# Kernel optimization log

Measured on AMD Instinct MI355X. Metric: run time of the kernel, lower is better.

Reference implementation:

```python
import jax, jax.numpy as jnp
import numpy as np

N_NODES = 100000


def gcn_conv(x, edge_index, W, b):
    # PyG GCNConv: add self-loops, symmetric norm, then scatter-aggregate.
    n = x.shape[0]
    x = x @ W  # [N, out]
    src = jnp.concatenate([edge_index[0], jnp.arange(n)])  # self-loops
    dst = jnp.concatenate([edge_index[1], jnp.arange(n)])
    ones = jnp.ones(src.shape[0], dtype=x.dtype)
    deg = jax.ops.segment_sum(ones, dst, num_segments=n)  # in-degree incl. self-loops
    dis = jnp.where(deg > 0, jax.lax.rsqrt(deg), 0.0)
    norm = dis[src] * dis[dst]  # [E+N]
    msg = x[src] * norm[:, None]  # gather + scale
    out = jax.ops.segment_sum(msg, dst, num_segments=n)
    return out + b


def setup_inputs() -> dict:
    key = jax.random.key(0)
    ks = jax.random.split(key, 8)
    in_dim, h1, h2, out_dim, E = 128, 128, 64, 10, 1600000
    glorot = lambda k, fi, fo: jax.random.normal(k, (fi, fo), jnp.float32) * np.sqrt(2.0 / (fi + fo))
    return {
        "x": jax.random.normal(ks[0], (N_NODES, in_dim), jnp.float32),
        "edge_index": jax.random.randint(ks[1], (2, E), 0, N_NODES, jnp.int64),
        "W1": glorot(ks[2], in_dim, h1),
        "b1": jnp.zeros((h1,), jnp.float32),
        "W2": glorot(ks[3], h1, h2),
        "b2": jnp.zeros((h2,), jnp.float32),
        "Wf": glorot(ks[4], h2, out_dim),
        "bf": jnp.zeros((out_dim,), jnp.float32),
    }


def reference(x, edge_index, W1, b1, W2, b2, Wf, bf):
    h = jax.nn.relu(gcn_conv(x, edge_index, W1, b1))
    h = jax.nn.relu(gcn_conv(h, edge_index, W2, b2))
    logits = h @ Wf + bf
    return jax.nn.softmax(logits, axis=1)
```

## Files before the change

### kernel.cpp

```cpp
#include <hip/hip_runtime.h>
#include <math.h>

#define NN 100000
#define D_IN 128
#define D_H1 128
#define D_H2 64
#define D_O 10
#define NB 256
#define BDIV 391
#define ECH 2048
#define COLCAP 8192

static const size_t OFF_G1     = 0;
static const size_t OFF_G2     = 25600000;
static const size_t OFF_PART   = 76800000;
static const size_t OFF_COL    = 102400000;
static const size_t OFF_DIS    = 108800000;
static const size_t OFF_ROWPTR = 109300000;
static const size_t OFF_HIST   = 109800000;
static const size_t OFF_TOT    = 110700000;
static const size_t OFF_BASE   = 110710000;

typedef __attribute__((ext_vector_type(8))) short short8;
typedef __attribute__((ext_vector_type(4))) float floatx4;

__device__ inline unsigned int pack_bf2(float a, float b) {
  unsigned int ua = __float_as_uint(a);
  ua += 0x7fffu + ((ua >> 16) & 1u);
  unsigned int ub = __float_as_uint(b);
  ub += 0x7fffu + ((ub >> 16) & 1u);
  return (ua >> 16) | (ub & 0xffff0000u);
}
__device__ inline unsigned short bf16u(float a) {
  unsigned int ua = __float_as_uint(a);
  ua += 0x7fffu + ((ua >> 16) & 1u);
  return (unsigned short)(ua >> 16);
}
__device__ inline float bflo(unsigned int u) { return __uint_as_float(u << 16); }
__device__ inline float bfhi(unsigned int u) { return __uint_as_float(u & 0xffff0000u); }
__device__ inline short8 as_short8(uint4 u) {
  union { uint4 u4; short8 s8; } c; c.u4 = u; return c.s8;
}
__device__ inline void acc_u4(float* acc, uint4 u) {
  acc[0] += bflo(u.x); acc[1] += bfhi(u.x);
  acc[2] += bflo(u.y); acc[3] += bfhi(u.y);
  acc[4] += bflo(u.z); acc[5] += bfhi(u.z);
  acc[6] += bflo(u.w); acc[7] += bfhi(u.w);
}

__global__ __launch_bounds__(256) void histo_kernel(
    const int* __restrict__ dst, int* __restrict__ H, int E, int nchunk) {
  __shared__ int hist[NB];
  const int tid = threadIdx.x;
  hist[tid] = 0;
  __syncthreads();
  const int e0 = blockIdx.x * ECH;
#pragma unroll
  for (int i = 0; i < ECH / 256; ++i) {
    int e = e0 + i * 256 + tid;
    if (e < E) atomicAdd(&hist[dst[e] / BDIV], 1);
  }
  __syncthreads();
  H[tid * nchunk + blockIdx.x] = hist[tid];
}

__global__ __launch_bounds__(256) void bucket_scan_kernel(
    int* __restrict__ H, int* __restrict__ total, int nchunk) {
  __shared__ int sm[256];
  const int tid = threadIdx.x;
  int* row = H + (size_t)blockIdx.x * nchunk;
  int carry = 0;
  for (int t0 = 0; t0 < nchunk; t0 += 256) {
    int idx = t0 + tid;
    int v = (idx < nchunk) ? row[idx] : 0;
    sm[tid] = v;
    __syncthreads();
#pragma unroll
    for (int off = 1; off < 256; off <<= 1) {
      int t2 = (tid >= off) ? sm[tid - off] : 0;
      __syncthreads();
      sm[tid] += t2;
      __syncthreads();
    }
    int incl = sm[tid];
    int ttot = sm[255];
    __syncthreads();
    if (idx < nchunk) row[idx] = carry + incl - v;
    carry += ttot;
  }
  if (tid == 0) total[blockIdx.x] = carry;
}

__global__ __launch_bounds__(256) void base_scan_kernel(
    const int* __restrict__ total, int* __restrict__ base) {
  __shared__ int sm[256];
  const int tid = threadIdx.x;
  int v = total[tid];
  sm[tid] = v;
  __syncthreads();
#pragma unroll
  for (int off = 1; off < 256; off <<= 1) {
    int t2 = (tid >= off) ? sm[tid - off] : 0;
    __syncthreads();
    sm[tid] += t2;
    __syncthreads();
  }
  base[tid] = sm[tid] - v;
  if (tid == 255) base[256] = sm[255];
}

__global__ __launch_bounds__(256) void scatter_kernel(
    const int* __restrict__ src, const int* __restrict__ dst,
    const int* __restrict__ H, const int* __restrict__ base,
    int2* __restrict__ part, int E, int nchunk) {
  __shared__ int offs_s[NB];
  __shared__ int base_s[NB];
  __shared__ int cnt[NB];
  const int tid = threadIdx.x;
  offs_s[tid] = H[tid * nchunk + blockIdx.x];
  base_s[tid] = base[tid];
  cnt[tid] = 0;
  __syncthreads();
  const int e0 = blockIdx.x * ECH;
#pragma unroll
  for (int i = 0; i < ECH / 256; ++i) {
    int e = e0 + i * 256 + tid;
    if (e < E) {
      int d = dst[e];
      int s = src[e];
      int b = d / BDIV;
      int r = atomicAdd(&cnt[b], 1);
      part[(size_t)base_s[b] + offs_s[b] + r] = make_int2(d, s);
    }
  }
}

__global__ __launch_bounds__(256) void bucket_csr_kernel(
    const int2* __restrict__ part, const int* __restrict__ base,
    int* __restrict__ row_ptr, float* __restrict__ dis,
    int* __restrict__ col, int n, int E) {
  __shared__ int sm[256];
  __shared__ int ldeg[BDIV + 1];
  __shared__ int lofs[BDIV + 1];
  __shared__ int col_s[COLCAP];
  const int tid = threadIdx.x;
  const int b = blockIdx.x;
  const int lo = b * BDIV;
  const int nn = min(n - lo, BDIV);
  const int ebase = base[b];
  const int ecnt = base[b + 1] - ebase;

  for (int t = tid; t <= BDIV; t += 256) ldeg[t] = 0;
  __syncthreads();
  for (int i0 = 0; i0 < ecnt; i0 += 256) {
    int idx = i0 + tid;
    if (idx < ecnt) atomicAdd(&ldeg[part[ebase + idx].x - lo], 1);
  }
  __syncthreads();
  int carry = 0;
  for (int t0 = 0; t0 < BDIV + 1; t0 += 256) {
    int idx = t0 + tid;
    int v = (idx <= BDIV) ? ldeg[idx] : 0;
    sm[tid] = v;
    __syncthreads();
#pragma unroll
    for (int off = 1; off < 256; off <<= 1) {
      int t2 = (tid >= off) ? sm[tid - off] : 0;
      __syncthreads();
      sm[tid] += t2;
      __syncthreads();
    }
    int incl = sm[tid];
    int ttot = sm[255];
    __syncthreads();
    if (idx <= BDIV) lofs[idx] = carry + incl - v;
    carry += ttot;
  }
  __syncthreads();
  for (int t = tid; t < nn; t += 256) {
    row_ptr[lo + t] = ebase + lofs[t];
    dis[lo + t] = rsqrtf((float)ldeg[t] + 1.0f);
  }
  if (b == NB - 1 && tid == 0) row_ptr[n] = E;
  __syncthreads();
  for (int i0 = 0; i0 < ecnt; i0 += 256) {
    int idx = i0 + tid;
    if (idx < ecnt) {
      int2 p = part[ebase + idx];
      int r = atomicAdd(&lofs[p.x - lo], 1);
      if (r < COLCAP) col_s[r] = p.y;
    }
  }
  __syncthreads();
  const int m = min(ecnt, COLCAP);
  for (int idx = tid; idx < m; idx += 256) col[ebase + idx] = col_s[idx];
}

template <int NOUT>
__global__ __launch_bounds__(256) void gemm_mfma_kernel(
    const float* __restrict__ A_, const float* __restrict__ W,
    const float* __restrict__ dis, unsigned short* __restrict__ out, int nrows) {
  constexpr int K = 128;
  constexpr int NT = NOUT / 16;
  constexpr int LDW = K + 8;
  __shared__ unsigned short wt[NOUT * LDW];
  __shared__ unsigned short buf[4 * 16 * LDW];
  const int tid = threadIdx.x;

  {
    constexpr int NGRP = 256 / NOUT;
    constexpr int KG = K / NGRP;
    int n = tid % NOUT;
    int k0 = (tid / NOUT) * KG;
#pragma unroll
    for (int kb = 0; kb < KG / 8; ++kb) {
      int k = k0 + kb * 8;
      unsigned int u0 = pack_bf2(W[(size_t)(k + 0) * NOUT + n], W[(size_t)(k + 1) * NOUT + n]);
      unsigned int u1 = pack_bf2(W[(size_t)(k + 2) * NOUT + n], W[(size_t)(k + 3) * NOUT + n]);
      unsigned int u2 = pack_bf2(W[(size_t)(k + 4) * NOUT + n], W[(size_t)(k + 5) * NOUT + n]);
      unsigned int u3 = pack_bf2(W[(size_t)(k + 6) * NOUT + n], W[(size_t)(k + 7) * NOUT + n]);
      *(uint4*)(wt + n * LDW + k) = make_uint4(u0, u1, u2, u3);
    }
  }

  const int wave = tid >> 6;
  const int lane = tid & 63;
  const int quad = lane >> 4;
  const int cg = lane & 15;
  const int row0w = blockIdx.x * 64 + wave * 16;

  short8 afr[4];
  {
    int row = row0w + cg;
    if (row > nrows - 1) row = nrows - 1;
#pragma unroll
    for (int kb = 0; kb < 4; ++kb) {
      const float* p = A_ + (size_t)row * K + kb * 32 + quad * 8;
      float4 v0 = *(const float4*)(p);
      float4 v1 = *(const float4*)(p + 4);
      uint4 u;
      u.x = pack_bf2(v0.x, v0.y); u.y = pack_bf2(v0.z, v0.w);
      u.z = pack_bf2(v1.x, v1.y); u.w = pack_bf2(v1.z, v1.w);
      afr[kb] = as_short8(u);
    }
  }
  __syncthreads();

  floatx4 acc[NT];
#pragma unroll
  for (int t = 0; t < NT; ++t) acc[t] = (floatx4){0.f, 0.f, 0.f, 0.f};
#pragma unroll
  for (int t = 0; t < NT; ++t) {
    const unsigned short* wrow = wt + (t * 16 + cg) * LDW;
#pragma unroll
    for (int kb = 0; kb < 4; ++kb) {
      short8 bfr = *(const short8*)(wrow + kb * 32 + quad * 8);
      acc[t] = __builtin_amdgcn_mfma_f32_16x16x32_bf16(afr[kb], bfr, acc[t], 0, 0, 0);
    }
  }

  float4 dv4 = *(const float4*)(dis + row0w + quad * 4);
  float dvs[4] = {dv4.x, dv4.y, dv4.z, dv4.w};
  unsigned short* mybuf = buf + wave * 16 * LDW;
#pragma unroll
  for (int t = 0; t < NT; ++t)
#pragma unroll
    for (int r = 0; r < 4; ++r)
      mybuf[(quad * 4 + r) * LDW + t * 16 + cg] = bf16u(acc[t][r] * dvs[r]);
  __syncthreads();

  constexpr int CHUNKS = NOUT / 8;
  constexpr int RPI = 64 / CHUNKS;
  int cid = lane % CHUNKS;
  int rs = lane / CHUNKS;
#pragma unroll
  for (int i = 0; i < 16 / RPI; ++i) {
    int r = rs + i * RPI;
    int grow = row0w + r;
    if (grow < nrows) {
      uint4 u = *(const uint4*)(mybuf + r * LDW + cid * 8);
      *(uint4*)(out + (size_t)grow * NOUT + cid * 8) = u;
    }
  }
}

__global__ __launch_bounds__(256) void gather1_gemm2_kernel(
    const unsigned short* __restrict__ g, const int* __restrict__ col,
    const int* __restrict__ row_ptr, const float* __restrict__ dis,
    const float* __restrict__ b1, const float* __restrict__ W2,
    unsigned short* __restrict__ g2, int n) {
  constexpr int K = D_H1;
  constexpr int LDW = K + 8;
  constexpr int LDO = 80;
  __shared__ unsigned short wt[D_H2 * LDW];
  __shared__ unsigned short hl[16 * LDW];
  __shared__ unsigned short obuf[16 * LDO];
  const int tid = threadIdx.x;
  const int row0 = blockIdx.x * 16;

  {
    int nn = tid & 63;
    int k0 = (tid >> 6) * 32;
#pragma unroll
    for (int kb = 0; kb < 4; ++kb) {
      int k = k0 + kb * 8;
      unsigned int u0 = pack_bf2(W2[(size_t)(k + 0) * D_H2 + nn], W2[(size_t)(k + 1) * D_H2 + nn]);
      unsigned int u1 = pack_bf2(W2[(size_t)(k + 2) * D_H2 + nn], W2[(size_t)(k + 3) * D_H2 + nn]);
      unsigned int u2 = pack_bf2(W2[(size_t)(k + 4) * D_H2 + nn], W2[(size_t)(k + 5) * D_H2 + nn]);
      unsigned int u3 = pack_bf2(W2[(size_t)(k + 6) * D_H2 + nn], W2[(size_t)(k + 7) * D_H2 + nn]);
      *(uint4*)(wt + nn * LDW + k) = make_uint4(u0, u1, u2, u3);
    }
  }

  {
    const int v = row0 + (tid >> 4);
    const int c = (tid & 15) * 8;
    const int start = row_ptr[v];
    const int end = row_ptr[v + 1];
    float acc[8];
#pragma unroll
    for (int q = 0; q < 8; ++q) acc[q] = 0.f;
    acc_u4(acc, *(const uint4*)(g + (size_t)v * K + c));
    int e = start;
    for (; e + 4 <= end; e += 4) {
      int s0 = col[e + 0], s1 = col[e + 1], s2 = col[e + 2], s3 = col[e + 3];
      uint4 u0 = *(const uint4*)(g + (size_t)s0 * K + c);
      uint4 u1 = *(const uint4*)(g + (size_t)s1 * K + c);
      uint4 u2 = *(const uint4*)(g + (size_t)s2 * K + c);
      uint4 u3 = *(const uint4*)(g + (size_t)s3 * K + c);
      acc_u4(acc, u0); acc_u4(acc, u1); acc_u4(acc, u2); acc_u4(acc, u3);
    }
    for (; e < end; ++e) {
      uint4 u = *(const uint4*)(g + (size_t)col[e] * K + c);
      acc_u4(acc, u);
    }
    float dv = dis[v];
    float4 bv0 = *(const float4*)(b1 + c);
    float4 bv1 = *(const float4*)(b1 + c + 4);
    float r0 = fmaxf(dv * acc[0] + bv0.x, 0.f);
    float r1 = fmaxf(dv * acc[1] + bv0.y, 0.f);
    float r2 = fmaxf(dv * acc[2] + bv0.z, 0.f);
    float r3 = fmaxf(dv * acc[3] + bv0.w, 0.f);
    float r4 = fmaxf(dv * acc[4] + bv1.x, 0.f);
    float r5 = fmaxf(dv * acc[5] + bv1.y, 0.f);
    float r6 = fmaxf(dv * acc[6] + bv1.z, 0.f);
    float r7 = fmaxf(dv * acc[7] + bv1.w, 0.f);
    uint4 o;
    o.x = pack_bf2(r0, r1);
    o.y = pack_bf2(r2, r3);
    o.z = pack_bf2(r4, r5);
    o.w = pack_bf2(r6, r7);
    *(uint4*)(hl + (tid >> 4) * LDW + c) = o;
  }
  __syncthreads();

  {
    const int wave = tid >> 6;
    const int lane = tid & 63;
    const int quad = lane >> 4;
    const int cg = lane & 15;
    floatx4 acc = (floatx4){0.f, 0.f, 0.f, 0.f};
    const unsigned short* wrow = wt + (wave * 16 + cg) * LDW;
    const unsigned short* arow = hl + cg * LDW;
#pragma unroll
    for (int kb = 0; kb < 4; ++kb) {
      short8 afr = *(const short8*)(arow + kb * 32 + quad * 8);
      short8 bfr = *(const short8*)(wrow + kb * 32 + quad * 8);
      acc = __builtin_amdgcn_mfma_f32_16x16x32_bf16(afr, bfr, acc, 0, 0, 0);
    }
    float4 dv4 = *(const float4*)(dis + row0 + quad * 4);
    float dvs[4] = {dv4.x, dv4.y, dv4.z, dv4.w};
#pragma unroll
    for (int r = 0; r < 4; ++r)
      obuf[(quad * 4 + r) * LDO + wave * 16 + cg] = bf16u(acc[r] * dvs[r]);
  }
  __syncthreads();

  if (tid < 128) {
    int r = tid >> 3;
    int cid = tid & 7;
    uint4 u = *(const uint4*)(obuf + r * LDO + cid * 8);
    *(uint4*)(g2 + (size_t)(row0 + r) * D_H2 + cid * 8) = u;
  }
}

__global__ __launch_bounds__(256) void gather2_final_kernel(
    const unsigned short* __restrict__ g, const int* __restrict__ col,
    const int* __restrict__ row_ptr, const float* __restrict__ dis,
    const float* __restrict__ b2, const float* __restrict__ Wf,
    const float* __restrict__ bf, float* __restrict__ out, int n) {
  constexpr int LDH = 72;
  __shared__ unsigned short ha[32 * LDH];
  __shared__ unsigned short wtf[16 * LDH];
  __shared__ float bfs[D_O];
  __shared__ float ls[32][12];
  const int tid = threadIdx.x;
  if (tid < 128) {
    int nn = tid >> 3;
    int k = (tid & 7) * 8;
    uint4 u;
    if (nn < D_O) {
      u.x = pack_bf2(Wf[(size_t)(k + 0) * D_O + nn], Wf[(size_t)(k + 1) * D_O + nn]);
      u.y = pack_bf2(Wf[(size_t)(k + 2) * D_O + nn], Wf[(size_t)(k + 3) * D_O + nn]);
      u.z = pack_bf2(Wf[(size_t)(k + 4) * D_O + nn], Wf[(size_t)(k + 5) * D_O + nn]);
      u.w = pack_bf2(Wf[(size_t)(k + 6) * D_O + nn], Wf[(size_t)(k + 7) * D_O + nn]);
    } else {
      u = make_uint4(0u, 0u, 0u, 0u);
    }
    *(uint4*)(wtf + nn * LDH + k) = u;
  }
  if (tid < D_O) bfs[tid] = bf[tid];

  const int gid = blockIdx.x * 256 + tid;
  const int v = gid >> 3;
  const int nl = tid >> 3;
  const int c = (tid & 7) * 8;
  if (v < n) {
    int start = row_ptr[v];
    int end = row_ptr[v + 1];
    float acc[8];
#pragma unroll
    for (int q = 0; q < 8; ++q) acc[q] = 0.f;
    acc_u4(acc, *(const uint4*)(g + (size_t)v * D_H2 + c));
    int e = start;
    for (; e + 4 <= end; e += 4) {
      int s0 = col[e + 0], s1 = col[e + 1], s2 = col[e + 2], s3 = col[e + 3];
      uint4 u0 = *(const uint4*)(g + (size_t)s0 * D_H2 + c);
      uint4 u1 = *(const uint4*)(g + (size_t)s1 * D_H2 + c);
      uint4 u2 = *(const uint4*)(g + (size_t)s2 * D_H2 + c);
      uint4 u3 = *(const uint4*)(g + (size_t)s3 * D_H2 + c);
      acc_u4(acc, u0); acc_u4(acc, u1); acc_u4(acc, u2); acc_u4(acc, u3);
    }
    for (; e < end; ++e) {
      uint4 u = *(const uint4*)(g + (size_t)col[e] * D_H2 + c);
      acc_u4(acc, u);
    }
    float dv = dis[v];
    float4 bv0 = *(const float4*)(b2 + c);
    float4 bv1 = *(const float4*)(b2 + c + 4);
    float r0 = fmaxf(dv * acc[0] + bv0.x, 0.f);
    float r1 = fmaxf(dv * acc[1] + bv0.y, 0.f);
    float r2 = fmaxf(dv * acc[2] + bv0.z, 0.f);
    float r3 = fmaxf(dv * acc[3] + bv0.w, 0.f);
    float r4 = fmaxf(dv * acc[4] + bv1.x, 0.f);
    float r5 = fmaxf(dv * acc[5] + bv1.y, 0.f);
    float r6 = fmaxf(dv * acc[6] + bv1.z, 0.f);
    float r7 = fmaxf(dv * acc[7] + bv1.w, 0.f);
    uint4 o;
    o.x = pack_bf2(r0, r1);
    o.y = pack_bf2(r2, r3);
    o.z = pack_bf2(r4, r5);
    o.w = pack_bf2(r6, r7);
    *(uint4*)(ha + nl * LDH + c) = o;
  }
  __syncthreads();
  {
    const int wave = tid >> 6;
    if (wave < 2) {
      const int lane = tid & 63;
      const int quad = lane >> 4;
      const int cg = lane & 15;
      floatx4 acc = (floatx4){0.f, 0.f, 0.f, 0.f};
      const unsigned short* arow = ha + (wave * 16 + cg) * LDH;
      const unsigned short* wrow = wtf + cg * LDH;
#pragma unroll
      for (int kb = 0; kb < 2; ++kb) {
        short8 afr = *(const short8*)(arow + kb * 32 + quad * 8);
        short8 bfr = *(const short8*)(wrow + kb * 32 + quad * 8);
        acc = __builtin_amdgcn_mfma_f32_16x16x32_bf16(afr, bfr, acc, 0, 0, 0);
      }
      if (cg < D_O) {
        float bb = bfs[cg];
#pragma unroll
        for (int r = 0; r < 4; ++r)
          ls[wave * 16 + quad * 4 + r][cg] = acc[r] + bb;
      }
    }
  }
  __syncthreads();
  if (tid < 32) {
    int v2 = blockIdx.x * 32 + tid;
    if (v2 < n) {
      float m = ls[tid][0];
#pragma unroll
      for (int j = 1; j < D_O; ++j) m = fmaxf(m, ls[tid][j]);
      float s = 0.f;
      float ex[D_O];
#pragma unroll
      for (int j = 0; j < D_O; ++j) { ex[j] = expf(ls[tid][j] - m); s += ex[j]; }
      float inv = 1.0f / s;
#pragma unroll
      for (int j = 0; j < D_O; ++j) ls[tid][j] = ex[j] * inv;
    }
  }
  __syncthreads();
  for (int idx = tid; idx < 32 * D_O; idx += 256) {
    int gidx = blockIdx.x * 32 * D_O + idx;
    if (gidx < n * D_O) out[gidx] = ls[idx / D_O][idx % D_O];
  }
}

extern "C" void kernel_launch(void* const* d_in, const int* in_sizes, int n_in,
                              void* d_out, int out_size, void* d_ws, size_t ws_size,
                              hipStream_t stream) {
  const float* x  = (const float*)d_in[0];
  const int*   ei = (const int*)d_in[1];
  const float* W1 = (const float*)d_in[2];
  const float* b1 = (const float*)d_in[3];
  const float* W2 = (const float*)d_in[4];
  const float* b2 = (const float*)d_in[5];
  const float* Wf = (const float*)d_in[6];
  const float* bf = (const float*)d_in[7];
  float* out = (float*)d_out;

  const int E = in_sizes[1] / 2;
  const int* src = ei;
  const int* dst = ei + E;

  char* ws = (char*)d_ws;
  unsigned short* g1 = (unsigned short*)(ws + OFF_G1);
  unsigned short* g2 = (unsigned short*)(ws + OFF_G2);
  int2*  part    = (int2*)(ws + OFF_PART);
  int*   col     = (int*)(ws + OFF_COL);
  float* dis     = (float*)(ws + OFF_DIS);
  int*   row_ptr = (int*)(ws + OFF_ROWPTR);
  int*   H       = (int*)(ws + OFF_HIST);
  int*   total   = (int*)(ws + OFF_TOT);
  int*   base    = (int*)(ws + OFF_BASE);

  const int nchunk = (E + ECH - 1) / ECH;

  histo_kernel<<<nchunk, 256, 0, stream>>>(dst, H, E, nchunk);
  bucket_scan_kernel<<<NB, 256, 0, stream>>>(H, total, nchunk);
  base_scan_kernel<<<1, 256, 0, stream>>>(total, base);
  scatter_kernel<<<nchunk, 256, 0, stream>>>(src, dst, H, base, part, E, nchunk);
  bucket_csr_kernel<<<NB, 256, 0, stream>>>(part, base, row_ptr, dis, col, NN, E);

  gemm_mfma_kernel<D_H1>
      <<<(NN + 63) / 64, 256, 0, stream>>>(x, W1, dis, g1, NN);

  gather1_gemm2_kernel<<<NN / 16, 256, 0, stream>>>(
      g1, col, row_ptr, dis, b1, W2, g2, NN);

  gather2_final_kernel<<<(NN + 31) / 32, 256, 0, stream>>>(
      g2, col, row_ptr, dis, b2, Wf, bf, out, NN);
}
```

Before: 251.4 us.

## Fold base scan into consumers, pack edge pairs into 32-bit words, double chunk size

Removes the single-block base_scan launch by recomputing the 256-entry prefix scan of bucket totals inside scatter and bucket_csr blocks. Packs each (local dst, src) pair into one 32-bit word (9-bit local dst, 17-bit src), halving the partition buffer traffic written by scatter and read twice by bucket_csr. Doubles the edge chunk per scatter/histogram block, reducing block count and histogram size. It adds redundant scan work in every block and relies on node ids fitting in 17 bits and bucket width under 512.

```diff
diff --git a/kernel.cpp b/kernel.cpp
--- a/kernel.cpp
+++ b/kernel.cpp
@@ -8,7 +8,7 @@
 #define D_O 10
 #define NB 256
 #define BDIV 391
-#define ECH 2048
+#define ECH 4096
 #define COLCAP 8192
 
 static const size_t OFF_G1     = 0;
@@ -19,7 +19,6 @@
 static const size_t OFF_ROWPTR = 109300000;
 static const size_t OFF_HIST   = 109800000;
 static const size_t OFF_TOT    = 110700000;
-static const size_t OFF_BASE   = 110710000;
 
 typedef __attribute__((ext_vector_type(8))) short short8;
 typedef __attribute__((ext_vector_type(4))) float floatx4;
@@ -91,34 +90,29 @@
   if (tid == 0) total[blockIdx.x] = carry;
 }
 
-__global__ __launch_bounds__(256) void base_scan_kernel(
-    const int* __restrict__ total, int* __restrict__ base) {
-  __shared__ int sm[256];
-  const int tid = threadIdx.x;
-  int v = total[tid];
-  sm[tid] = v;
-  __syncthreads();
-#pragma unroll
-  for (int off = 1; off < 256; off <<= 1) {
-    int t2 = (tid >= off) ? sm[tid - off] : 0;
-    __syncthreads();
-    sm[tid] += t2;
-    __syncthreads();
-  }
-  base[tid] = sm[tid] - v;
-  if (tid == 255) base[256] = sm[255];
-}
-
 __global__ __launch_bounds__(256) void scatter_kernel(
     const int* __restrict__ src, const int* __restrict__ dst,
-    const int* __restrict__ H, const int* __restrict__ base,
-    int2* __restrict__ part, int E, int nchunk) {
+    const int* __restrict__ H, const int* __restrict__ total,
+    unsigned int* __restrict__ part, int E, int nchunk) {
+  __shared__ int sm[NB];
   __shared__ int offs_s[NB];
   __shared__ int base_s[NB];
   __shared__ int cnt[NB];
   const int tid = threadIdx.x;
+  {
+    int v = total[tid];
+    sm[tid] = v;
+    __syncthreads();
+#pragma unroll
+    for (int off = 1; off < 256; off <<= 1) {
+      int t2 = (tid >= off) ? sm[tid - off] : 0;
+      __syncthreads();
+      sm[tid] += t2;
+      __syncthreads();
+    }
+    base_s[tid] = sm[tid] - v;
+  }
   offs_s[tid] = H[tid * nchunk + blockIdx.x];
-  base_s[tid] = base[tid];
   cnt[tid] = 0;
   __syncthreads();
   const int e0 = blockIdx.x * ECH;
@@ -130,31 +124,45 @@
       int s = src[e];
       int b = d / BDIV;
       int r = atomicAdd(&cnt[b], 1);
-      part[(size_t)base_s[b] + offs_s[b] + r] = make_int2(d, s);
+      unsigned int p = ((unsigned int)(d - b * BDIV) << 17) | (unsigned int)s;
+      part[(size_t)base_s[b] + offs_s[b] + r] = p;
     }
   }
 }
 
 __global__ __launch_bounds__(256) void bucket_csr_kernel(
-    const int2* __restrict__ part, const int* __restrict__ base,
+    const unsigned int* __restrict__ part, const int* __restrict__ total,
     int* __restrict__ row_ptr, float* __restrict__ dis,
     int* __restrict__ col, int n, int E) {
   __shared__ int sm[256];
   __shared__ int ldeg[BDIV + 1];
   __shared__ int lofs[BDIV + 1];
   __shared__ int col_s[COLCAP];
+  __shared__ int ebase_s, ecnt_s;
   const int tid = threadIdx.x;
   const int b = blockIdx.x;
   const int lo = b * BDIV;
   const int nn = min(n - lo, BDIV);
-  const int ebase = base[b];
-  const int ecnt = base[b + 1] - ebase;
-
+  {
+    int v = total[tid];
+    sm[tid] = v;
+    __syncthreads();
+#pragma unroll
+    for (int off = 1; off < 256; off <<= 1) {
+      int t2 = (tid >= off) ? sm[tid - off] : 0;
+      __syncthreads();
+      sm[tid] += t2;
+      __syncthreads();
+    }
+    if (tid == b) { ebase_s = sm[tid] - v; ecnt_s = v; }
+  }
   for (int t = tid; t <= BDIV; t += 256) ldeg[t] = 0;
   __syncthreads();
+  const int ebase = ebase_s;
+  const int ecnt = ecnt_s;
   for (int i0 = 0; i0 < ecnt; i0 += 256) {
     int idx = i0 + tid;
-    if (idx < ecnt) atomicAdd(&ldeg[part[ebase + idx].x - lo], 1);
+    if (idx < ecnt) atomicAdd(&ldeg[part[ebase + idx] >> 17], 1);
   }
   __syncthreads();
   int carry = 0;
@@ -186,9 +194,9 @@
   for (int i0 = 0; i0 < ecnt; i0 += 256) {
     int idx = i0 + tid;
     if (idx < ecnt) {
-      int2 p = part[ebase + idx];
-      int r = atomicAdd(&lofs[p.x - lo], 1);
-      if (r < COLCAP) col_s[r] = p.y;
+      unsigned int p = part[ebase + idx];
+      int r = atomicAdd(&lofs[p >> 17], 1);
+      if (r < COLCAP) col_s[r] = (int)(p & 0x1FFFFu);
     }
   }
   __syncthreads();
@@ -520,21 +528,19 @@
   char* ws = (char*)d_ws;
   unsigned short* g1 = (unsigned short*)(ws + OFF_G1);
   unsigned short* g2 = (unsigned short*)(ws + OFF_G2);
-  int2*  part    = (int2*)(ws + OFF_PART);
+  unsigned int* part = (unsigned int*)(ws + OFF_PART);
   int*   col     = (int*)(ws + OFF_COL);
   float* dis     = (float*)(ws + OFF_DIS);
   int*   row_ptr = (int*)(ws + OFF_ROWPTR);
   int*   H       = (int*)(ws + OFF_HIST);
   int*   total   = (int*)(ws + OFF_TOT);
-  int*   base    = (int*)(ws + OFF_BASE);
 
   const int nchunk = (E + ECH - 1) / ECH;
 
   histo_kernel<<<nchunk, 256, 0, stream>>>(dst, H, E, nchunk);
   bucket_scan_kernel<<<NB, 256, 0, stream>>>(H, total, nchunk);
-  base_scan_kernel<<<1, 256, 0, stream>>>(total, base);
-  scatter_kernel<<<nchunk, 256, 0, stream>>>(src, dst, H, base, part, E, nchunk);
-  bucket_csr_kernel<<<NB, 256, 0, stream>>>(part, base, row_ptr, dis, col, NN, E);
+  scatter_kernel<<<nchunk, 256, 0, stream>>>(src, dst, H, total, part, E, nchunk);
+  bucket_csr_kernel<<<NB, 256, 0, stream>>>(part, total, row_ptr, dis, col, NN, E);
 
   gemm_mfma_kernel<D_H1>
       <<<(NN + 63) / 64, 256, 0, stream>>>(x, W1, dis, g1, NN);
```

Result: faster. 244.7 us (-2.7%).
